# Kernel tuning notes

Measured on AMD Instinct MI355X. Metric: run time of the kernel, lower is better.

## Reference

```python
import jax, jax.numpy as jnp
import numpy as np

GAMMA = 2.0  # init arg gamma
EPS = 1e-8   # torch F.cosine_similarity eps


def setup_inputs() -> dict:
    key = jax.random.key(0)
    k1, k2, k3 = jax.random.split(key, 3)
    B, C, H, W_ = 4, 256, 64, 64
    x = jax.random.normal(k1, (B, C, H, W_), dtype=jnp.float32)
    # 1x1 conv weight [out_c, in_c] and bias
    W = jax.random.normal(k2, (C, C), dtype=jnp.float32) * (1.0 / np.sqrt(C))
    b = jax.random.normal(k3, (C,), dtype=jnp.float32) * 0.01
    return {"x": x, "W": W, "b": b}


def reference(x, W, b):
    B, C, H, W_ = x.shape
    N = H * W_
    xf = x.reshape(B, C, N)                                    # [B,C,N]
    # cosine similarity across channel dim, with torch-style eps clamp
    norm = jnp.maximum(jnp.sqrt(jnp.sum(xf * xf, axis=1)), EPS)  # [B,N]
    xn = xf / norm[:, None, :]                                  # [B,C,N]
    sim = jnp.einsum('bcn,bcm->bnm', xn, xn)                    # [B,N,N]
    sim = jax.nn.relu(sim) ** GAMMA
    # 1x1 conv = per-pixel channel mixing
    t = jnp.einsum('oc,bchw->bohw', W, x) + b[None, :, None, None]
    tf = t.reshape(B, C, N)                                     # [B,C,N]
    # einsum 'b x y h w, b c h w -> b c x y'
    out = jnp.einsum('bnm,bcm->bcn', sim, tf)
    return out.reshape(B, C, H, W_)
```

## Files before the change

### kernel.cpp

```cpp
#include <hip/hip_runtime.h>
#include <stdint.h>

#define CC 256
#define NN 4096

typedef __attribute__((ext_vector_type(8))) short short8;
typedef __attribute__((ext_vector_type(4))) float floatx4;
typedef __attribute__((ext_vector_type(4))) unsigned int uint4v;
typedef __attribute__((ext_vector_type(2))) unsigned int uint2v;

__device__ __forceinline__ unsigned short f2bf(float f) {
    unsigned int u = __builtin_bit_cast(unsigned int, f);
    u = (u + 0x7FFFu + ((u >> 16) & 1u)) >> 16;
    return (unsigned short)u;
}

__device__ __forceinline__ floatx4 mfma16(short8 a, short8 b, floatx4 c) {
    return __builtin_amdgcn_mfma_f32_16x16x32_bf16(a, b, c, 0, 0, 0);
}


__global__ __launch_bounds__(256) void k_trans(const float* __restrict__ x,
                                               unsigned short* __restrict__ xB,
                                               unsigned short* __restrict__ xG,
                                               float* __restrict__ psum) {
    int blk = blockIdx.x;
    int b  = blk >> 8;
    int cc = (blk >> 6) & 3;
    int nc = blk & 63;
    int c0 = cc << 6, n0 = nc << 6;
    __shared__ float tile[64][65];
    __shared__ float red[4][64];
    int t = threadIdx.x;
    {
        int c   = t >> 2;
        int nn4 = (t & 3) << 4;
        const float* src = x + (size_t)(b * CC + c0 + c) * NN + n0 + nn4;
        #pragma unroll
        for (int j = 0; j < 16; j += 4) {
            floatx4 v = *(const floatx4*)(src + j);
            tile[c][nn4 + j + 0] = v[0];
            tile[c][nn4 + j + 1] = v[1];
            tile[c][nn4 + j + 2] = v[2];
            tile[c][nn4 + j + 3] = v[3];
        }
    }
    __syncthreads();
    int g = t >> 6, lane = t & 63, l15 = lane & 15, q = lane >> 4;
    #pragma unroll
    for (int kkl = 0; kkl < 2; ++kkl) {
        unsigned int w[4];
        #pragma unroll
        for (int j = 0; j < 4; ++j) {
            unsigned int lo = f2bf(tile[32 * kkl + 8 * q + 2 * j][16 * g + l15]);
            unsigned int hi = f2bf(tile[32 * kkl + 8 * q + 2 * j + 1][16 * g + l15]);
            w[j] = lo | (hi << 16);
        }
        uint4v p = {w[0], w[1], w[2], w[3]};
        *(uint4v*)(xB + ((size_t)(b * 256 + (n0 >> 4) + g) * 8 + (c0 >> 5) + kkl) * 512
                   + lane * 8) = p;
    }
    #pragma unroll
    for (int kk2 = 0; kk2 < 2; ++kk2) {
        unsigned int w[4];
        #pragma unroll
        for (int j = 0; j < 4; ++j) {
            unsigned int lo = f2bf(tile[16 * g + l15][32 * kk2 + 8 * q + 2 * j]);
            unsigned int hi = f2bf(tile[16 * g + l15][32 * kk2 + 8 * q + 2 * j + 1]);
            w[j] = lo | (hi << 16);
        }
        uint4v p = {w[0], w[1], w[2], w[3]};
        *(uint4v*)(xG + (size_t)(b * 64 + nc) * 16 * 1024
                   + ((size_t)((c0 >> 4) + g)) * 1024 + kk2 * 512 + lane * 8) = p;
    }
    {
        int n  = t & 63;
        int cq = t >> 6;
        float ss = 0.f;
        #pragma unroll
        for (int i = 0; i < 16; ++i) {
            float v = tile[cq * 16 + i][n];
            ss = fmaf(v, v, ss);
        }
        red[cq][n] = ss;
    }
    __syncthreads();
    if (t < 64) {
        float s = red[0][t] + red[1][t] + red[2][t] + red[3][t];
        psum[((size_t)(b * 64 + nc) * 64 + t) * 4 + cc] = s;
    }
}

__global__ __launch_bounds__(256) void k_invwcast(const float* __restrict__ psum,
                                                  float* __restrict__ invn,
                                                  const float* __restrict__ Wm,
                                                  unsigned short* __restrict__ wF) {
    int bid = blockIdx.x;
    int t = threadIdx.x;
    if (bid < 64) {
        int i = bid * 256 + t;
        floatx4 p = *(const floatx4*)(psum + (size_t)i * 4);
        float ss = (p[0] + p[1]) + (p[2] + p[3]);
        invn[i] = 1.f / fmaxf(sqrtf(ss), 1e-8f);
    } else {
        int idx = (bid - 64) * 256 + t;
        int f = idx >> 6, lane = idx & 63;
        int ct = f >> 3, kk = f & 7;
        int l15 = lane & 15, q = lane >> 4;
        const float* src = Wm + (size_t)(16 * ct + l15) * CC + 32 * kk + 8 * q;
        floatx4 a = *(const floatx4*)src;
        floatx4 c = *(const floatx4*)(src + 4);
        unsigned int w0 = f2bf(a[0]) | ((unsigned int)f2bf(a[1]) << 16);
        unsigned int w1 = f2bf(a[2]) | ((unsigned int)f2bf(a[3]) << 16);
        unsigned int w2 = f2bf(c[0]) | ((unsigned int)f2bf(c[1]) << 16);
        unsigned int w3 = f2bf(c[2]) | ((unsigned int)f2bf(c[3]) << 16);
        uint4v p = {w0, w1, w2, w3};
        *(uint4v*)(wF + (size_t)f * 512 + lane * 8) = p;
    }
}

#define FUSED_STEP(IT, BQC, BQN, XGP, XGC, DO_G2)                              \
    {                                                                          \
                \
        _Pragma("unroll")                                                      \
        for (int kk = 0; kk < 8; ++kk)                                         \
            BQN[kk] = *(const short8*)(bqp + kk * 512);                        \
        bqp += 16384;                                                          \
        _Pragma("unroll")                                                      \
        for (int ci = 0; ci < 2; ++ci)                                         \
            _Pragma("unroll")                                                  \
            for (int kk2 = 0; kk2 < 2; ++kk2)                                  \
                XGC[ci][kk2] = *(const short8*)(xgp + ci * 8192 + kk2 * 512);  \
        xgp += 16384;                                                          \
        floatx4 invm4 = *(const floatx4*)invmp;                                \
        invmp += 64;                                                           \
                                       \
        if (DO_G2) {                                                           \
            const unsigned short* pbR = pbuf[((IT) - 1) & 1];                  \
            _Pragma("unroll")                                                  \
            for (int kk2 = 0; kk2 < 2; ++kk2)                                  \
                _Pragma("unroll")                                              \
                for (int nqs = 0; nqs < 4; ++nqs) {                            \
                    short8 pbf = *(const short8*)(pbR + (16 * nqs + l15) * 72  \
                                                  + kk2 * 32 + q * 8);         \
                    Zacc[0][nqs] = mfma16(XGP[0][kk2], pbf, Zacc[0][nqs]);     \
                    Zacc[1][nqs] = mfma16(XGP[1][kk2], pbf, Zacc[1][nqs]);     \
                }                                                              \
        }                                                                      \
                  \
        floatx4 s0a = zero4, s0b = zero4, s1a = zero4, s1b = zero4;            \
        _Pragma("unroll")                                                      \
        for (int kk = 0; kk < 8; kk += 2) {                                    \
            s0a = mfma16(BQC[kk],     aq[0][kk],     s0a);                     \
            s1a = mfma16(BQC[kk],     aq[1][kk],     s1a);                     \
            s0b = mfma16(BQC[kk + 1], aq[0][kk + 1], s0b);                     \
            s1b = mfma16(BQC[kk + 1], aq[1][kk + 1], s1b);                     \
        }                                                                      \
                  \
        {                                                                      \
            unsigned short* pbW = pbuf[(IT) & 1];                              \
            _Pragma("unroll")                                                  \
            for (int s = 0; s < 2; ++s) {                                      \
                floatx4 sv = (s == 0) ? (s0a + s0b) : (s1a + s1b);             \
                unsigned int pk0, pk1;                                         \
                float v0 = sv[0] * (invm4[0] * invq[s]);                       \
                float v1 = sv[1] * (invm4[1] * invq[s]);                       \
                float v2 = sv[2] * (invm4[2] * invq[s]);                       \
                float v3 = sv[3] * (invm4[3] * invq[s]);                       \
                v0 = fmaxf(v0, 0.f); v1 = fmaxf(v1, 0.f);                      \
                v2 = fmaxf(v2, 0.f); v3 = fmaxf(v3, 0.f);                      \
                v0 *= v0; v1 *= v1; v2 *= v2; v3 *= v3;                        \
                csum[s] += (v0 + v1) + (v2 + v3);                              \
                pk0 = __byte_perm(__builtin_bit_cast(unsigned int, v0) + 0x8000u, \
                                  __builtin_bit_cast(unsigned int, v1) + 0x8000u, \
                                  0x7632);                                     \
                pk1 = __byte_perm(__builtin_bit_cast(unsigned int, v2) + 0x8000u, \
                                  __builtin_bit_cast(unsigned int, v3) + 0x8000u, \
                                  0x7632);                                     \
                uint2v w2 = {pk0, pk1};                                        \
                *(uint2v*)(pbW + (16 * (2 * np + s) + l15) * 72                \
                           + 16 * ms + 4 * q) = w2;                            \
            }                                                                  \
        }                                                                      \
        asm volatile("s_waitcnt lgkmcnt(0)\n\ts_barrier" ::: "memory");        \
    }

__global__ __launch_bounds__(512, 1) void k_fused(
        const unsigned short* __restrict__ xB,
        const unsigned short* __restrict__ xG,
        const unsigned short* __restrict__ wF,
        const float* __restrict__ bias,
        const float* __restrict__ invn,
        float* __restrict__ out) {
    int blk = blockIdx.x;
    int b  = blk >> 6;
    int n0 = (blk & 63) << 6;
    int t  = threadIdx.x;
    int wv = t >> 6, lane = t & 63;
    int l15 = lane & 15, q = lane >> 4;
    int ms = wv & 3;
    int np = wv >> 2;

    __shared__ unsigned short pbuf[2][64 * 72];
    __shared__ unsigned short zbuf[64 * 264];
    __shared__ float spbuf2[4][64];

    const unsigned short* xBb = xB + (size_t)b * 256 * 8 * 512;
    const unsigned short* xGb = xG + (size_t)b * 64 * 16 * 1024;
    const float* invb = invn + b * NN;

    short8 aq[2][8];
    #pragma unroll
    for (int s = 0; s < 2; ++s)
        #pragma unroll
        for (int kk = 0; kk < 8; ++kk)
            aq[s][kk] = *(const short8*)(xBb
                + ((size_t)((n0 >> 4) + 2 * np + s) * 8 + kk) * 512 + lane * 8);
    float invq[2];
    #pragma unroll
    for (int s = 0; s < 2; ++s) invq[s] = invb[n0 + 16 * (2 * np + s) + l15];

    floatx4 zero4 = {0.f, 0.f, 0.f, 0.f};
    floatx4 Zacc[2][4];
    #pragma unroll
    for (int ci = 0; ci < 2; ++ci)
        #pragma unroll
        for (int nqs = 0; nqs < 4; ++nqs) Zacc[ci][nqs] = zero4;
    float csum[2] = {0.f, 0.f};

    const unsigned short* bqp   = xBb + ms * 4096 + lane * 8;
    const unsigned short* xgp   = xGb + wv * 1024 + lane * 8;
    const float*          invmp = invb + 16 * ms + 4 * q;

    short8 bqA[8], bqB[8];
    short8 xgA[2][2], xgB[2][2];
    #pragma unroll
    for (int kk = 0; kk < 8; ++kk)
        bqA[kk] = *(const short8*)(bqp + kk * 512);
    bqp += 16384;

    FUSED_STEP(0, bqA, bqB, xgB, xgA, false)
    for (int it2 = 0; it2 < 31; ++it2) {
        int itO = 2 * it2 + 1;
        FUSED_STEP(itO, bqB, bqA, xgA, xgB, true)
        int itE = 2 * it2 + 2;
        FUSED_STEP(itE, bqA, bqB, xgB, xgA, true)
    }
    FUSED_STEP(63, bqB, bqA, xgA, xgB, true)
    {
        const unsigned short* pbR = pbuf[1];
        #pragma unroll
        for (int kk2 = 0; kk2 < 2; ++kk2)
            #pragma unroll
            for (int nqs = 0; nqs < 4; ++nqs) {
                short8 pbf = *(const short8*)(pbR + (16 * nqs + l15) * 72
                                              + kk2 * 32 + q * 8);
                Zacc[0][nqs] = mfma16(xgB[0][kk2], pbf, Zacc[0][nqs]);
                Zacc[1][nqs] = mfma16(xgB[1][kk2], pbf, Zacc[1][nqs]);
            }
    }

    #pragma unroll
    for (int s = 0; s < 2; ++s) {
        csum[s] += __shfl_xor(csum[s], 16, 64);
        csum[s] += __shfl_xor(csum[s], 32, 64);
    }

    __syncthreads();
    #pragma unroll
    for (int ci = 0; ci < 2; ++ci) {
        int cct = wv + 8 * ci;
        #pragma unroll
        for (int nqs = 0; nqs < 4; ++nqs)
            #pragma unroll
            for (int i = 0; i < 4; ++i)
                zbuf[(16 * nqs + l15) * 264 + 16 * cct + 4 * q + i] = f2bf(Zacc[ci][nqs][i]);
    }
    if (q == 0) {
        #pragma unroll
        for (int s = 0; s < 2; ++s)
            spbuf2[ms][16 * (2 * np + s) + l15] = csum[s];
    }
    __syncthreads();

    float svals[4];
    #pragma unroll
    for (int nqs = 0; nqs < 4; ++nqs)
        svals[nqs] = spbuf2[0][16 * nqs + l15] + spbuf2[1][16 * nqs + l15]
                   + spbuf2[2][16 * nqs + l15] + spbuf2[3][16 * nqs + l15];

    float* ob = out + (size_t)b * CC * NN;
    floatx4 oa[2][4];
    #pragma unroll
    for (int ci = 0; ci < 2; ++ci) {
        int ct = wv + 8 * ci;
        floatx4 bv = *(const floatx4*)(bias + 16 * ct + 4 * q);
        #pragma unroll
        for (int nqs = 0; nqs < 4; ++nqs)
            #pragma unroll
            for (int i = 0; i < 4; ++i) oa[ci][nqs][i] = bv[i] * svals[nqs];
    }
    #pragma unroll
    for (int kk = 0; kk < 8; ++kk) {
        short8 wf0 = *(const short8*)(wF + (size_t)(wv * 8 + kk) * 512 + lane * 8);
        short8 wf1 = *(const short8*)(wF + (size_t)((wv + 8) * 8 + kk) * 512 + lane * 8);
        #pragma unroll
        for (int nqs = 0; nqs < 4; ++nqs) {
            short8 zf = *(const short8*)(&zbuf[(16 * nqs + l15) * 264 + 32 * kk + 8 * q]);
            oa[0][nqs] = mfma16(wf0, zf, oa[0][nqs]);
            oa[1][nqs] = mfma16(wf1, zf, oa[1][nqs]);
        }
    }
    #pragma unroll
    for (int ci = 0; ci < 2; ++ci) {
        int ct = wv + 8 * ci;
        #pragma unroll
        for (int nqs = 0; nqs < 4; ++nqs)
            #pragma unroll
            for (int i = 0; i < 4; ++i)
                ob[(size_t)(16 * ct + 4 * q + i) * NN + n0 + 16 * nqs + l15] = oa[ci][nqs][i];
    }
}

extern "C" void kernel_launch(void* const* d_in, const int* in_sizes, int n_in,
                              void* d_out, int out_size, void* d_ws, size_t ws_size,
                              hipStream_t stream) {
    const float* x    = (const float*)d_in[0];
    const float* Wm   = (const float*)d_in[1];
    const float* bias = (const float*)d_in[2];
    float* out = (float*)d_out;

    char* ws = (char*)d_ws;
    float* psum         = (float*)ws;
    float* invn         = (float*)(ws + 262144);
    unsigned short* xB  = (unsigned short*)(ws + 262144 + 65536);
    unsigned short* xG  = (unsigned short*)(ws + 262144 + 65536 + 8388608);
    unsigned short* wF  = (unsigned short*)(ws + 262144 + 65536 + 2 * 8388608);

    k_trans   <<<1024, 256, 0, stream>>>(x, xB, xG, psum);
    k_invwcast<<<96,   256, 0, stream>>>(psum, invn, Wm, wF);
    k_fused   <<<256,  512, 0, stream>>>(xB, xG, wF, bias, invn, out);
}
```

Measured before the change: 152.3 us.

## Process two key tiles per barrier with doubled P buffers and setprio

The fused loop now handles two 64-column key tiles per barrier, using a two-level P buffer in shared memory. This halves the number of block-wide barriers. Loads of the next B tiles move to after each substep's MFMA and softmax-like work, and s_setprio raises wave priority around the MFMA sections to encourage overlap. The block-to-(batch, query-tile) mapping is also remapped so that neighbouring blocks interleave batches, likely for cache or XCD locality. The cost is more registers for the doubled xG fragments and more LDS.

```diff
diff --git a/kernel.cpp b/kernel.cpp
--- a/kernel.cpp
+++ b/kernel.cpp
@@ -119,54 +119,40 @@
     }
 }
 
-#define FUSED_STEP(IT, BQC, BQN, XGP, XGC, DO_G2)                              \
+#define SUBSTEP(SETW, EO, BQ, XGP, INV, DO_G2)                                 \
     {                                                                          \
-                \
-        _Pragma("unroll")                                                      \
-        for (int kk = 0; kk < 8; ++kk)                                         \
-            BQN[kk] = *(const short8*)(bqp + kk * 512);                        \
-        bqp += 16384;                                                          \
-        _Pragma("unroll")                                                      \
-        for (int ci = 0; ci < 2; ++ci)                                         \
-            _Pragma("unroll")                                                  \
-            for (int kk2 = 0; kk2 < 2; ++kk2)                                  \
-                XGC[ci][kk2] = *(const short8*)(xgp + ci * 8192 + kk2 * 512);  \
-        xgp += 16384;                                                          \
-        floatx4 invm4 = *(const floatx4*)invmp;                                \
-        invmp += 64;                                                           \
-                                       \
+        __builtin_amdgcn_s_setprio(1);                                         \
         if (DO_G2) {                                                           \
-            const unsigned short* pbR = pbuf[((IT) - 1) & 1];                  \
+            const unsigned short* pbR = pbuf[1 - (SETW)][EO];                  \
             _Pragma("unroll")                                                  \
             for (int kk2 = 0; kk2 < 2; ++kk2)                                  \
                 _Pragma("unroll")                                              \
                 for (int nqs = 0; nqs < 4; ++nqs) {                            \
                     short8 pbf = *(const short8*)(pbR + (16 * nqs + l15) * 72  \
                                                   + kk2 * 32 + q * 8);         \
-                    Zacc[0][nqs] = mfma16(XGP[0][kk2], pbf, Zacc[0][nqs]);     \
-                    Zacc[1][nqs] = mfma16(XGP[1][kk2], pbf, Zacc[1][nqs]);     \
+                    Zacc[0][nqs] = mfma16(XGP[EO][0][kk2], pbf, Zacc[0][nqs]); \
+                    Zacc[1][nqs] = mfma16(XGP[EO][1][kk2], pbf, Zacc[1][nqs]); \
                 }                                                              \
         }                                                                      \
-                  \
         floatx4 s0a = zero4, s0b = zero4, s1a = zero4, s1b = zero4;            \
         _Pragma("unroll")                                                      \
         for (int kk = 0; kk < 8; kk += 2) {                                    \
-            s0a = mfma16(BQC[kk],     aq[0][kk],     s0a);                     \
-            s1a = mfma16(BQC[kk],     aq[1][kk],     s1a);                     \
-            s0b = mfma16(BQC[kk + 1], aq[0][kk + 1], s0b);                     \
-            s1b = mfma16(BQC[kk + 1], aq[1][kk + 1], s1b);                     \
+            s0a = mfma16(BQ[kk],     aq[0][kk],     s0a);                      \
+            s1a = mfma16(BQ[kk],     aq[1][kk],     s1a);                      \
+            s0b = mfma16(BQ[kk + 1], aq[0][kk + 1], s0b);                      \
+            s1b = mfma16(BQ[kk + 1], aq[1][kk + 1], s1b);                      \
         }                                                                      \
-                  \
+        __builtin_amdgcn_s_setprio(0);                                         \
         {                                                                      \
-            unsigned short* pbW = pbuf[(IT) & 1];                              \
+            unsigned short* pbW = pbuf[SETW][EO];                              \
             _Pragma("unroll")                                                  \
             for (int s = 0; s < 2; ++s) {                                      \
                 floatx4 sv = (s == 0) ? (s0a + s0b) : (s1a + s1b);             \
                 unsigned int pk0, pk1;                                         \
-                float v0 = sv[0] * (invm4[0] * invq[s]);                       \
-                float v1 = sv[1] * (invm4[1] * invq[s]);                       \
-                float v2 = sv[2] * (invm4[2] * invq[s]);                       \
-                float v3 = sv[3] * (invm4[3] * invq[s]);                       \
+                float v0 = sv[0] * (INV[0] * invq[s]);                         \
+                float v1 = sv[1] * (INV[1] * invq[s]);                         \
+                float v2 = sv[2] * (INV[2] * invq[s]);                         \
+                float v3 = sv[3] * (INV[3] * invq[s]);                         \
                 v0 = fmaxf(v0, 0.f); v1 = fmaxf(v1, 0.f);                      \
                 v2 = fmaxf(v2, 0.f); v3 = fmaxf(v3, 0.f);                      \
                 v0 *= v0; v1 *= v1; v2 *= v2; v3 *= v3;                        \
@@ -182,6 +168,29 @@
                            + 16 * ms + 4 * q) = w2;                            \
             }                                                                  \
         }                                                                      \
+        _Pragma("unroll")                                                      \
+        for (int kk = 0; kk < 8; ++kk)                                         \
+            BQ[kk] = *(const short8*)(bqp + kk * 512);                         \
+        bqp += 16384;                                                          \
+    }
+
+#define STEP2(SETW, XGP, XGC, DO_G2)                                           \
+    {                                                                          \
+                  \
+        _Pragma("unroll")                                                      \
+        for (int eo = 0; eo < 2; ++eo)                                         \
+            _Pragma("unroll")                                                  \
+            for (int ci = 0; ci < 2; ++ci)                                     \
+                _Pragma("unroll")                                              \
+                for (int kk2 = 0; kk2 < 2; ++kk2)                              \
+                    XGC[eo][ci][kk2] = *(const short8*)(xgp + eo * 16384       \
+                                                       + ci * 8192 + kk2 * 512); \
+        xgp += 32768;                                                          \
+        floatx4 invE = *(const floatx4*)invmp;                                 \
+        floatx4 invO = *(const floatx4*)(invmp + 64);                          \
+        invmp += 128;                                                          \
+        SUBSTEP(SETW, 0, bqE, XGP, invE, DO_G2)                                \
+        SUBSTEP(SETW, 1, bqO, XGP, invO, DO_G2)                                \
         asm volatile("s_waitcnt lgkmcnt(0)\n\ts_barrier" ::: "memory");        \
     }
 
@@ -193,15 +202,16 @@
         const float* __restrict__ invn,
         float* __restrict__ out) {
     int blk = blockIdx.x;
-    int b  = blk >> 6;
-    int n0 = (blk & 63) << 6;
+    int b  = (blk & 7) >> 1;
+    int qt = ((blk >> 3) << 1) | (blk & 1);
+    int n0 = qt << 6;
     int t  = threadIdx.x;
     int wv = t >> 6, lane = t & 63;
     int l15 = lane & 15, q = lane >> 4;
     int ms = wv & 3;
     int np = wv >> 2;
 
-    __shared__ unsigned short pbuf[2][64 * 72];
+    __shared__ unsigned short pbuf[2][2][64 * 72];
     __shared__ unsigned short zbuf[64 * 264];
     __shared__ float spbuf2[4][64];
 
@@ -232,31 +242,34 @@
     const unsigned short* xgp   = xGb + wv * 1024 + lane * 8;
     const float*          invmp = invb + 16 * ms + 4 * q;
 
-    short8 bqA[8], bqB[8];
-    short8 xgA[2][2], xgB[2][2];
+    short8 bqE[8], bqO[8];
+    short8 xgA[2][2][2], xgB[2][2][2];
     #pragma unroll
     for (int kk = 0; kk < 8; ++kk)
-        bqA[kk] = *(const short8*)(bqp + kk * 512);
+        bqE[kk] = *(const short8*)(bqp + kk * 512);
     bqp += 16384;
-
-    FUSED_STEP(0, bqA, bqB, xgB, xgA, false)
-    for (int it2 = 0; it2 < 31; ++it2) {
-        int itO = 2 * it2 + 1;
-        FUSED_STEP(itO, bqB, bqA, xgA, xgB, true)
-        int itE = 2 * it2 + 2;
-        FUSED_STEP(itE, bqA, bqB, xgB, xgA, true)
-    }
-    FUSED_STEP(63, bqB, bqA, xgA, xgB, true)
-    {
-        const unsigned short* pbR = pbuf[1];
+    #pragma unroll
+    for (int kk = 0; kk < 8; ++kk)
+        bqO[kk] = *(const short8*)(bqp + kk * 512);
+    bqp += 16384;
+
+    STEP2(0, xgB, xgA, false)
+    for (int t2 = 0; t2 < 15; ++t2) {
+        STEP2(1, xgA, xgB, true)
+        STEP2(0, xgB, xgA, true)
+    }
+    STEP2(1, xgA, xgB, true)
+    #pragma unroll
+    for (int eo = 0; eo < 2; ++eo) {
+        const unsigned short* pbR = pbuf[1][eo];
         #pragma unroll
         for (int kk2 = 0; kk2 < 2; ++kk2)
             #pragma unroll
             for (int nqs = 0; nqs < 4; ++nqs) {
                 short8 pbf = *(const short8*)(pbR + (16 * nqs + l15) * 72
                                               + kk2 * 32 + q * 8);
-                Zacc[0][nqs] = mfma16(xgB[0][kk2], pbf, Zacc[0][nqs]);
-                Zacc[1][nqs] = mfma16(xgB[1][kk2], pbf, Zacc[1][nqs]);
+                Zacc[0][nqs] = mfma16(xgB[eo][0][kk2], pbf, Zacc[0][nqs]);
+                Zacc[1][nqs] = mfma16(xgB[eo][1][kk2], pbf, Zacc[1][nqs]);
             }
     }
 
```

New measurement: 186.0 us. +22.1%, slower.
